# Kernel tuning notes

Hardware: AMD Instinct MI355X
Metric: run time of the kernel (lower is better)

## Reference

```python
import jax, jax.numpy as jnp
import numpy as np

EPSILON = 1e-8
DT = 0.1
STEPS = 3
MASK_DENSITY = 0.01


def setup_inputs() -> dict:
    key = jax.random.key(0)
    k1, k2 = jax.random.split(key)
    B, S, D = 4, 4096, 2
    psi = jax.random.normal(k1, (B, S, D), dtype=jnp.float32)
    # binary mask: threshold a uniform draw to get a sparse 0/1 adjacency
    u = jax.random.uniform(k2, (B, S, S), dtype=jnp.float32)
    binary_mask = (u < MASK_DENSITY).astype(jnp.float32)
    return {"psi": psi, "binary_mask": binary_mask}


def reference(psi, binary_mask):
    def force(state):
        # adjacency-weighted aggregation minus self: [B,S,S] @ [B,S,2]
        return jnp.einsum('bij,bjd->bid', binary_mask, state) - state

    def step(p, _):
        r = jnp.linalg.norm(p, axis=-1, keepdims=True)          # [B,S,1]
        k1 = force(p)
        psi_star = p + DT * k1
        star_norm = jnp.linalg.norm(psi_star, axis=-1, keepdims=True)
        psi_star = psi_star * (r / (star_norm + EPSILON))       # renormalize to r
        k2 = force(psi_star)
        p_new = p + 0.5 * DT * (k1 + k2)
        new_norm = jnp.linalg.norm(p_new, axis=-1, keepdims=True)
        p_new = p_new * (r / (new_norm + EPSILON))              # norm-preserving
        return p_new, None

    psi_out, _ = jax.lax.scan(step, psi, None, length=STEPS)
    return psi_out
```

## Files before the change

### kernel.cpp

```cpp
#include <hip/hip_runtime.h>
#include <stdint.h>

#define BATCH   4
#define SEQ     4096
#define WPR     64
#define NROWS   (BATCH * SEQ)
#define DTS     0.1f
#define HALF_DT 0.05f
#define EPS     1e-8f

__global__ void compress_mask(const float* __restrict__ mask,
                              unsigned long long* __restrict__ bits) {
    int w = blockIdx.x * blockDim.x + threadIdx.x;
    const float4* src = reinterpret_cast<const float4*>(mask) + (size_t)w * 16;
    unsigned long long acc = 0ull;
#pragma unroll
    for (int it = 0; it < 16; ++it) {
        float4 v = src[it];
        unsigned long long n =
              (unsigned long long)(v.x != 0.f)
            | ((unsigned long long)(v.y != 0.f) << 1)
            | ((unsigned long long)(v.z != 0.f) << 2)
            | ((unsigned long long)(v.w != 0.f) << 3);
        acc |= n << (it * 4);
    }
    bits[w] = acc;
}

template <int PHASE>
__global__ void force_step(const unsigned long long* __restrict__ bits,
                           const float2* __restrict__ pIn,
                           const float2* __restrict__ gsrc,
                           float2* __restrict__ k1buf,
                           float2* __restrict__ starbuf,
                           float*  __restrict__ rbuf,
                           float2* __restrict__ outbuf) {
    const int wave = threadIdx.x >> 6;
    const int lane = threadIdx.x & 63;
    const int row  = blockIdx.x * (blockDim.x >> 6) + wave;
    const int b    = row >> 12;
    const float2* gb = gsrc + ((size_t)b << 12);

    unsigned long long w = bits[(size_t)row * WPR + lane];
    float sx = 0.f, sy = 0.f;
    const int base = lane << 6;
    while (w) {
        int j = __builtin_ctzll(w);
        w &= (w - 1);
        float2 v = gb[base + j];
        sx += v.x; sy += v.y;
    }
#pragma unroll
    for (int m = 32; m >= 1; m >>= 1) {
        sx += __shfl_xor(sx, m, 64);
        sy += __shfl_xor(sy, m, 64);
    }
    if (lane == 0) {
        if (PHASE == 0) {
            float2 p = pIn[row];
            float r   = sqrtf(p.x * p.x + p.y * p.y);
            float k1x = sx - p.x, k1y = sy - p.y;
            float tx  = p.x + DTS * k1x, ty = p.y + DTS * k1y;
            float sc  = r / (sqrtf(tx * tx + ty * ty) + EPS);
            k1buf[row]   = make_float2(k1x, k1y);
            starbuf[row] = make_float2(tx * sc, ty * sc);
            rbuf[row]    = r;
        } else {
            float2 st = gsrc[row];
            float k2x = sx - st.x, k2y = sy - st.y;
            float2 p  = pIn[row];
            float2 k1 = k1buf[row];
            float nx  = p.x + HALF_DT * (k1.x + k2x);
            float ny  = p.y + HALF_DT * (k1.y + k2y);
            float sc  = rbuf[row] / (sqrtf(nx * nx + ny * ny) + EPS);
            outbuf[row] = make_float2(nx * sc, ny * sc);
        }
    }
}

extern "C" void kernel_launch(void* const* d_in, const int* in_sizes, int n_in,
                              void* d_out, int out_size, void* d_ws, size_t ws_size,
                              hipStream_t stream) {
    const float* psi  = (const float*)d_in[0];
    const float* mask = (const float*)d_in[1];
    float2* out2 = (float2*)d_out;

    char* ws = (char*)d_ws;
    unsigned long long* bits = (unsigned long long*)ws;
    float2* p    = (float2*)(ws + (size_t)NROWS * WPR * 8);
    float2* k1   = p + NROWS;
    float2* star = k1 + NROWS;
    float*  rbuf = (float*)(star + NROWS);

    compress_mask<<<NROWS * WPR / 256, 256, 0, stream>>>(mask, bits);

    const float2* psi2 = (const float2*)psi;
    const int fgrid = NROWS / 4;

    force_step<0><<<fgrid, 256, 0, stream>>>(bits, psi2, psi2, k1, star, rbuf, nullptr);
    force_step<1><<<fgrid, 256, 0, stream>>>(bits, psi2, star, k1, star, rbuf, p);
    force_step<0><<<fgrid, 256, 0, stream>>>(bits, p, p, k1, star, rbuf, nullptr);
    force_step<1><<<fgrid, 256, 0, stream>>>(bits, p, star, k1, star, rbuf, p);
    force_step<0><<<fgrid, 256, 0, stream>>>(bits, p, p, k1, star, rbuf, nullptr);
    force_step<1><<<fgrid, 256, 0, stream>>>(bits, p, star, k1, star, rbuf, out2);
}
```

Measured before the change: 407.3 us.

## Fuse mask compression and all RK steps into one cooperative kernel

Replaces the separate mask-compression kernel and the six force-step launches with one persistent cooperative kernel. Phases are separated by grid-wide syncs, and each wave handles four rows. Mask compression now has lanes read consecutive float4s (coalesced) and builds the bit words with wave ballots, which interleaves the column bit layout; the gather indexing is updated to match. This targets launch overhead and the strided, uncoalesced mask reads of the old compressor. The cost is grid-sync latency and a dependence on all 1024 blocks being co-resident.

```diff
diff --git a/kernel.cpp b/kernel.cpp
--- a/kernel.cpp
+++ b/kernel.cpp
@@ -1,5 +1,8 @@
 #include <hip/hip_runtime.h>
+#include <hip/hip_cooperative_groups.h>
 #include <stdint.h>
+
+namespace cg = cooperative_groups;
 
 #define BATCH   4
 #define SEQ     4096
@@ -9,45 +12,21 @@
 #define HALF_DT 0.05f
 #define EPS     1e-8f
 
-__global__ void compress_mask(const float* __restrict__ mask,
-                              unsigned long long* __restrict__ bits) {
-    int w = blockIdx.x * blockDim.x + threadIdx.x;
-    const float4* src = reinterpret_cast<const float4*>(mask) + (size_t)w * 16;
-    unsigned long long acc = 0ull;
-#pragma unroll
-    for (int it = 0; it < 16; ++it) {
-        float4 v = src[it];
-        unsigned long long n =
-              (unsigned long long)(v.x != 0.f)
-            | ((unsigned long long)(v.y != 0.f) << 1)
-            | ((unsigned long long)(v.z != 0.f) << 2)
-            | ((unsigned long long)(v.w != 0.f) << 3);
-        acc |= n << (it * 4);
-    }
-    bits[w] = acc;
-}
+#define NBLOCK  1024
+#define NTHR    256
+#define NWAVES  (NBLOCK * NTHR / 64)
+#define ROWS_PER_WAVE (NROWS / NWAVES)
 
-template <int PHASE>
-__global__ void force_step(const unsigned long long* __restrict__ bits,
-                           const float2* __restrict__ pIn,
-                           const float2* __restrict__ gsrc,
-                           float2* __restrict__ k1buf,
-                           float2* __restrict__ starbuf,
-                           float*  __restrict__ rbuf,
-                           float2* __restrict__ outbuf) {
-    const int wave = threadIdx.x >> 6;
-    const int lane = threadIdx.x & 63;
-    const int row  = blockIdx.x * (blockDim.x >> 6) + wave;
-    const int b    = row >> 12;
-    const float2* gb = gsrc + ((size_t)b << 12);
-
+__device__ __forceinline__ float2 row_force_sum(
+        const unsigned long long* __restrict__ bits,
+        const float2* __restrict__ gbatch, int row, int lane) {
     unsigned long long w = bits[(size_t)row * WPR + lane];
+    const int colbase = ((lane >> 2) << 8) | (lane & 3);
     float sx = 0.f, sy = 0.f;
-    const int base = lane << 6;
     while (w) {
         int j = __builtin_ctzll(w);
         w &= (w - 1);
-        float2 v = gb[base + j];
+        float2 v = gbatch[colbase + (j << 2)];
         sx += v.x; sy += v.y;
     }
 #pragma unroll
@@ -55,25 +34,81 @@
         sx += __shfl_xor(sx, m, 64);
         sy += __shfl_xor(sy, m, 64);
     }
-    if (lane == 0) {
-        if (PHASE == 0) {
+    return make_float2(sx, sy);
+}
+
+__global__ __launch_bounds__(NTHR, 4)
+void fused_rdi(const float* __restrict__ mask,
+               const float2* __restrict__ psi,
+               unsigned long long* __restrict__ bits,
+               float2* __restrict__ pbuf,
+               float2* __restrict__ k1buf,
+               float2* __restrict__ starbuf,
+               float*  __restrict__ rbuf,
+               float2* __restrict__ out) {
+    cg::grid_group grid = cg::this_grid();
+    const int wave = (blockIdx.x * NTHR + threadIdx.x) >> 6;
+    const int lane = threadIdx.x & 63;
+
+    for (int i = 0; i < ROWS_PER_WAVE; ++i) {
+        const int row = wave * ROWS_PER_WAVE + i;
+        const float4* src = reinterpret_cast<const float4*>(mask + (size_t)row * SEQ);
+        unsigned long long word = 0ull;
+#pragma unroll
+        for (int c = 0; c < 16; ++c) {
+            float4 v = src[c * 64 + lane];
+            unsigned long long b;
+            b = __ballot(v.x != 0.f); word = (lane == c * 4 + 0) ? b : word;
+            b = __ballot(v.y != 0.f); word = (lane == c * 4 + 1) ? b : word;
+            b = __ballot(v.z != 0.f); word = (lane == c * 4 + 2) ? b : word;
+            b = __ballot(v.w != 0.f); word = (lane == c * 4 + 3) ? b : word;
+        }
+        bits[(size_t)row * WPR + lane] = word;
+    }
+
+    __threadfence();
+    grid.sync();
+
+    for (int s = 0; s < 3; ++s) {
+        const float2* pIn  = (s == 0) ? psi : pbuf;
+        float2*       pOut = (s == 2) ? out : pbuf;
+
+        for (int i = 0; i < ROWS_PER_WAVE; ++i) {
+            const int row = wave * ROWS_PER_WAVE + i;
+            const int b = row >> 12;
+            float2 sum = row_force_sum(bits, pIn + ((size_t)b << 12), row, lane);
             float2 p = pIn[row];
             float r   = sqrtf(p.x * p.x + p.y * p.y);
-            float k1x = sx - p.x, k1y = sy - p.y;
+            float k1x = sum.x - p.x, k1y = sum.y - p.y;
             float tx  = p.x + DTS * k1x, ty = p.y + DTS * k1y;
             float sc  = r / (sqrtf(tx * tx + ty * ty) + EPS);
-            k1buf[row]   = make_float2(k1x, k1y);
-            starbuf[row] = make_float2(tx * sc, ty * sc);
-            rbuf[row]    = r;
-        } else {
-            float2 st = gsrc[row];
-            float k2x = sx - st.x, k2y = sy - st.y;
+            if (lane == 0) {
+                k1buf[row]   = make_float2(k1x, k1y);
+                starbuf[row] = make_float2(tx * sc, ty * sc);
+                rbuf[row]    = r;
+            }
+        }
+
+        __threadfence();
+        grid.sync();
+
+        for (int i = 0; i < ROWS_PER_WAVE; ++i) {
+            const int row = wave * ROWS_PER_WAVE + i;
+            const int b = row >> 12;
+            float2 sum = row_force_sum(bits, starbuf + ((size_t)b << 12), row, lane);
+            float2 st = starbuf[row];
             float2 p  = pIn[row];
             float2 k1 = k1buf[row];
+            float k2x = sum.x - st.x, k2y = sum.y - st.y;
             float nx  = p.x + HALF_DT * (k1.x + k2x);
             float ny  = p.y + HALF_DT * (k1.y + k2y);
             float sc  = rbuf[row] / (sqrtf(nx * nx + ny * ny) + EPS);
-            outbuf[row] = make_float2(nx * sc, ny * sc);
+            if (lane == 0) pOut[row] = make_float2(nx * sc, ny * sc);
+        }
+
+        if (s < 2) {
+            __threadfence();
+            grid.sync();
         }
     }
 }
@@ -92,15 +127,10 @@
     float2* star = k1 + NROWS;
     float*  rbuf = (float*)(star + NROWS);
 
-    compress_mask<<<NROWS * WPR / 256, 256, 0, stream>>>(mask, bits);
+    const float2* psi2 = (const float2*)psi;
 
-    const float2* psi2 = (const float2*)psi;
-    const int fgrid = NROWS / 4;
-
-    force_step<0><<<fgrid, 256, 0, stream>>>(bits, psi2, psi2, k1, star, rbuf, nullptr);
-    force_step<1><<<fgrid, 256, 0, stream>>>(bits, psi2, star, k1, star, rbuf, p);
-    force_step<0><<<fgrid, 256, 0, stream>>>(bits, p, p, k1, star, rbuf, nullptr);
-    force_step<1><<<fgrid, 256, 0, stream>>>(bits, p, star, k1, star, rbuf, p);
-    force_step<0><<<fgrid, 256, 0, stream>>>(bits, p, p, k1, star, rbuf, nullptr);
-    force_step<1><<<fgrid, 256, 0, stream>>>(bits, p, star, k1, star, rbuf, out2);
+    void* args[] = { (void*)&mask, (void*)&psi2, (void*)&bits, (void*)&p,
+                     (void*)&k1, (void*)&star, (void*)&rbuf, (void*)&out2 };
+    hipLaunchCooperativeKernel((void*)fused_rdi, dim3(NBLOCK), dim3(NTHR),
+                               args, 0, stream);
 }
```

Measured after the change: 1.565 ms. +284.3%, slower.

## Fuse mask compression with first force phase using wave-ballot bitpacking

Applied to the files above, without the earlier changes.

Mask compression now runs one wave per row. Each lane reads coalesced float4 chunks, and __ballot builds the 64-bit words, which gives an interleaved column layout. That kernel also computes the first phase-0 force step straight from the fresh bit words, so one launch and one reread of the bit matrix are gone. The gather index mapping changes to match the strided bit layout, which spreads each lane's neighbour reads across the row instead of a contiguous 64-column block.

```diff
diff --git a/kernel.cpp b/kernel.cpp
--- a/kernel.cpp
+++ b/kernel.cpp
@@ -9,45 +9,15 @@
 #define HALF_DT 0.05f
 #define EPS     1e-8f
 
-__global__ void compress_mask(const float* __restrict__ mask,
-                              unsigned long long* __restrict__ bits) {
-    int w = blockIdx.x * blockDim.x + threadIdx.x;
-    const float4* src = reinterpret_cast<const float4*>(mask) + (size_t)w * 16;
-    unsigned long long acc = 0ull;
-#pragma unroll
-    for (int it = 0; it < 16; ++it) {
-        float4 v = src[it];
-        unsigned long long n =
-              (unsigned long long)(v.x != 0.f)
-            | ((unsigned long long)(v.y != 0.f) << 1)
-            | ((unsigned long long)(v.z != 0.f) << 2)
-            | ((unsigned long long)(v.w != 0.f) << 3);
-        acc |= n << (it * 4);
-    }
-    bits[w] = acc;
-}
-
-template <int PHASE>
-__global__ void force_step(const unsigned long long* __restrict__ bits,
-                           const float2* __restrict__ pIn,
-                           const float2* __restrict__ gsrc,
-                           float2* __restrict__ k1buf,
-                           float2* __restrict__ starbuf,
-                           float*  __restrict__ rbuf,
-                           float2* __restrict__ outbuf) {
-    const int wave = threadIdx.x >> 6;
-    const int lane = threadIdx.x & 63;
-    const int row  = blockIdx.x * (blockDim.x >> 6) + wave;
-    const int b    = row >> 12;
-    const float2* gb = gsrc + ((size_t)b << 12);
-
-    unsigned long long w = bits[(size_t)row * WPR + lane];
+__device__ __forceinline__ float2 ballot_force_sum(unsigned long long w,
+                                                   const float2* __restrict__ gb,
+                                                   int lane) {
+    const int colbase = ((lane >> 2) << 8) | (lane & 3);
     float sx = 0.f, sy = 0.f;
-    const int base = lane << 6;
     while (w) {
         int j = __builtin_ctzll(w);
         w &= (w - 1);
-        float2 v = gb[base + j];
+        float2 v = gb[colbase + (j << 2)];
         sx += v.x; sy += v.y;
     }
 #pragma unroll
@@ -55,11 +25,67 @@
         sx += __shfl_xor(sx, m, 64);
         sy += __shfl_xor(sy, m, 64);
     }
+    return make_float2(sx, sy);
+}
+
+__global__ __launch_bounds__(256)
+void compress_phaseA(const float* __restrict__ mask,
+                     const float2* __restrict__ psi,
+                     unsigned long long* __restrict__ bits,
+                     float2* __restrict__ k1buf,
+                     float2* __restrict__ starbuf,
+                     float*  __restrict__ rbuf) {
+    const int row  = (blockIdx.x * blockDim.x + threadIdx.x) >> 6;
+    const int lane = threadIdx.x & 63;
+
+    const float4* src = reinterpret_cast<const float4*>(mask + (size_t)row * SEQ);
+    unsigned long long word = 0ull;
+#pragma unroll
+    for (int c = 0; c < 16; ++c) {
+        float4 v = src[c * 64 + lane];
+        unsigned long long b;
+        b = __ballot(v.x != 0.f); if (lane == c * 4 + 0) word = b;
+        b = __ballot(v.y != 0.f); if (lane == c * 4 + 1) word = b;
+        b = __ballot(v.z != 0.f); if (lane == c * 4 + 2) word = b;
+        b = __ballot(v.w != 0.f); if (lane == c * 4 + 3) word = b;
+    }
+    bits[(size_t)row * WPR + lane] = word;
+
+    const int bidx = row >> 12;
+    float2 sum = ballot_force_sum(word, psi + ((size_t)bidx << 12), lane);
+    float2 p  = psi[row];
+    float r   = sqrtf(p.x * p.x + p.y * p.y);
+    float k1x = sum.x - p.x, k1y = sum.y - p.y;
+    float tx  = p.x + DTS * k1x, ty = p.y + DTS * k1y;
+    float sc  = r / (sqrtf(tx * tx + ty * ty) + EPS);
+    if (lane == 0) {
+        k1buf[row]   = make_float2(k1x, k1y);
+        starbuf[row] = make_float2(tx * sc, ty * sc);
+        rbuf[row]    = r;
+    }
+}
+
+template <int PHASE>
+__global__ __launch_bounds__(256)
+void force_step(const unsigned long long* __restrict__ bits,
+                const float2* __restrict__ pIn,
+                const float2* __restrict__ gsrc,
+                float2* __restrict__ k1buf,
+                float2* __restrict__ starbuf,
+                float*  __restrict__ rbuf,
+                float2* __restrict__ outbuf) {
+    const int row  = (blockIdx.x * blockDim.x + threadIdx.x) >> 6;
+    const int lane = threadIdx.x & 63;
+    const int bidx = row >> 12;
+
+    unsigned long long w = bits[(size_t)row * WPR + lane];
+    float2 sum = ballot_force_sum(w, gsrc + ((size_t)bidx << 12), lane);
+
     if (lane == 0) {
         if (PHASE == 0) {
             float2 p = pIn[row];
             float r   = sqrtf(p.x * p.x + p.y * p.y);
-            float k1x = sx - p.x, k1y = sy - p.y;
+            float k1x = sum.x - p.x, k1y = sum.y - p.y;
             float tx  = p.x + DTS * k1x, ty = p.y + DTS * k1y;
             float sc  = r / (sqrtf(tx * tx + ty * ty) + EPS);
             k1buf[row]   = make_float2(k1x, k1y);
@@ -67,7 +93,7 @@
             rbuf[row]    = r;
         } else {
             float2 st = gsrc[row];
-            float k2x = sx - st.x, k2y = sy - st.y;
+            float k2x = sum.x - st.x, k2y = sum.y - st.y;
             float2 p  = pIn[row];
             float2 k1 = k1buf[row];
             float nx  = p.x + HALF_DT * (k1.x + k2x);
@@ -92,15 +118,13 @@
     float2* star = k1 + NROWS;
     float*  rbuf = (float*)(star + NROWS);
 
-    compress_mask<<<NROWS * WPR / 256, 256, 0, stream>>>(mask, bits);
+    const float2* psi2 = (const float2*)psi;
+    const int grid = NROWS / 4;
 
-    const float2* psi2 = (const float2*)psi;
-    const int fgrid = NROWS / 4;
-
-    force_step<0><<<fgrid, 256, 0, stream>>>(bits, psi2, psi2, k1, star, rbuf, nullptr);
-    force_step<1><<<fgrid, 256, 0, stream>>>(bits, psi2, star, k1, star, rbuf, p);
-    force_step<0><<<fgrid, 256, 0, stream>>>(bits, p, p, k1, star, rbuf, nullptr);
-    force_step<1><<<fgrid, 256, 0, stream>>>(bits, p, star, k1, star, rbuf, p);
-    force_step<0><<<fgrid, 256, 0, stream>>>(bits, p, p, k1, star, rbuf, nullptr);
-    force_step<1><<<fgrid, 256, 0, stream>>>(bits, p, star, k1, star, rbuf, out2);
+    compress_phaseA<<<grid, 256, 0, stream>>>(mask, psi2, bits, k1, star, rbuf);
+    force_step<1><<<grid, 256, 0, stream>>>(bits, psi2, star, k1, star, rbuf, p);
+    force_step<0><<<grid, 256, 0, stream>>>(bits, p, p, k1, star, rbuf, nullptr);
+    force_step<1><<<grid, 256, 0, stream>>>(bits, p, star, k1, star, rbuf, p);
+    force_step<0><<<grid, 256, 0, stream>>>(bits, p, p, k1, star, rbuf, nullptr);
+    force_step<1><<<grid, 256, 0, stream>>>(bits, p, star, k1, star, rbuf, out2);
 }
```

Measured after the change: 394.2 us. 1.03x faster.

## Coalesce mask compression with wave ballots and interleaved bit layout

Applied to the files above, without the earlier changes.

The mask compression kernel now has each wave read 64 consecutive float4s with fully coalesced loads and build the bitmask words with ballots, instead of each thread reading 16 strided float4s. The bit layout changes so each word covers interleaved columns, and force_step decodes column indices to match. Per-row operand loads in force_step are also hoisted ahead of the gather loop. The mask read dominates runtime, so coalescing it targets memory bandwidth, at the cost of more scattered gathers in the force kernels.

```diff
diff --git a/kernel.cpp b/kernel.cpp
--- a/kernel.cpp
+++ b/kernel.cpp
@@ -9,45 +9,61 @@
 #define HALF_DT 0.05f
 #define EPS     1e-8f
 
-__global__ void compress_mask(const float* __restrict__ mask,
-                              unsigned long long* __restrict__ bits) {
-    int w = blockIdx.x * blockDim.x + threadIdx.x;
-    const float4* src = reinterpret_cast<const float4*>(mask) + (size_t)w * 16;
-    unsigned long long acc = 0ull;
-#pragma unroll
-    for (int it = 0; it < 16; ++it) {
-        float4 v = src[it];
-        unsigned long long n =
-              (unsigned long long)(v.x != 0.f)
-            | ((unsigned long long)(v.y != 0.f) << 1)
-            | ((unsigned long long)(v.z != 0.f) << 2)
-            | ((unsigned long long)(v.w != 0.f) << 3);
-        acc |= n << (it * 4);
+#define CB_BLOCKS 2048
+#define CB_THR    256
+#define CB_WAVES  (CB_BLOCKS * CB_THR / 64)
+#define TOTAL_CHUNKS (NROWS * 16)
+#define CHUNKS_PER_WAVE (TOTAL_CHUNKS / CB_WAVES)
+
+__global__ __launch_bounds__(CB_THR)
+void compress_mask(const float* __restrict__ mask,
+                   unsigned long long* __restrict__ bits) {
+    const int wid  = (blockIdx.x * CB_THR + threadIdx.x) >> 6;
+    const int lane = threadIdx.x & 63;
+    const float4* m4 = reinterpret_cast<const float4*>(mask);
+
+#pragma unroll 8
+    for (int it = 0; it < CHUNKS_PER_WAVE; ++it) {
+        const int W = wid * CHUNKS_PER_WAVE + it;
+        float4 v = m4[(size_t)W * 64 + lane];
+        unsigned long long b0 = __ballot(v.x != 0.f);
+        unsigned long long b1 = __ballot(v.y != 0.f);
+        unsigned long long b2 = __ballot(v.z != 0.f);
+        unsigned long long b3 = __ballot(v.w != 0.f);
+        unsigned long long w01 = (lane & 1) ? b1 : b0;
+        unsigned long long w23 = (lane & 1) ? b3 : b2;
+        unsigned long long ws  = (lane & 2) ? w23 : w01;
+        if (lane < 4) bits[((size_t)W << 2) + lane] = ws;
     }
-    bits[w] = acc;
 }
 
 template <int PHASE>
-__global__ void force_step(const unsigned long long* __restrict__ bits,
-                           const float2* __restrict__ pIn,
-                           const float2* __restrict__ gsrc,
-                           float2* __restrict__ k1buf,
-                           float2* __restrict__ starbuf,
-                           float*  __restrict__ rbuf,
-                           float2* __restrict__ outbuf) {
-    const int wave = threadIdx.x >> 6;
+__global__ __launch_bounds__(256)
+void force_step(const unsigned long long* __restrict__ bits,
+                const float2* __restrict__ pIn,
+                const float2* __restrict__ gsrc,
+                float2* __restrict__ k1buf,
+                float2* __restrict__ starbuf,
+                float*  __restrict__ rbuf,
+                float2* __restrict__ outbuf) {
+    const int row  = (blockIdx.x * blockDim.x + threadIdx.x) >> 6;
     const int lane = threadIdx.x & 63;
-    const int row  = blockIdx.x * (blockDim.x >> 6) + wave;
-    const int b    = row >> 12;
-    const float2* gb = gsrc + ((size_t)b << 12);
+    const int bidx = row >> 12;
+    const float2* gb = gsrc + ((size_t)bidx << 12);
 
     unsigned long long w = bits[(size_t)row * WPR + lane];
+
+    float2 p = pIn[row];
+    float2 st = make_float2(0.f, 0.f), k1v = make_float2(0.f, 0.f);
+    float rr = 0.f;
+    if (PHASE == 1) { st = gsrc[row]; k1v = k1buf[row]; rr = rbuf[row]; }
+
+    const int colbase = ((lane >> 2) << 8) | (lane & 3);
     float sx = 0.f, sy = 0.f;
-    const int base = lane << 6;
     while (w) {
         int j = __builtin_ctzll(w);
         w &= (w - 1);
-        float2 v = gb[base + j];
+        float2 v = gb[colbase + (j << 2)];
         sx += v.x; sy += v.y;
     }
 #pragma unroll
@@ -55,9 +71,9 @@
         sx += __shfl_xor(sx, m, 64);
         sy += __shfl_xor(sy, m, 64);
     }
+
     if (lane == 0) {
         if (PHASE == 0) {
-            float2 p = pIn[row];
             float r   = sqrtf(p.x * p.x + p.y * p.y);
             float k1x = sx - p.x, k1y = sy - p.y;
             float tx  = p.x + DTS * k1x, ty = p.y + DTS * k1y;
@@ -66,13 +82,10 @@
             starbuf[row] = make_float2(tx * sc, ty * sc);
             rbuf[row]    = r;
         } else {
-            float2 st = gsrc[row];
             float k2x = sx - st.x, k2y = sy - st.y;
-            float2 p  = pIn[row];
-            float2 k1 = k1buf[row];
-            float nx  = p.x + HALF_DT * (k1.x + k2x);
-            float ny  = p.y + HALF_DT * (k1.y + k2y);
-            float sc  = rbuf[row] / (sqrtf(nx * nx + ny * ny) + EPS);
+            float nx  = p.x + HALF_DT * (k1v.x + k2x);
+            float ny  = p.y + HALF_DT * (k1v.y + k2y);
+            float sc  = rr / (sqrtf(nx * nx + ny * ny) + EPS);
             outbuf[row] = make_float2(nx * sc, ny * sc);
         }
     }
@@ -92,10 +105,10 @@
     float2* star = k1 + NROWS;
     float*  rbuf = (float*)(star + NROWS);
 
-    compress_mask<<<NROWS * WPR / 256, 256, 0, stream>>>(mask, bits);
-
     const float2* psi2 = (const float2*)psi;
     const int fgrid = NROWS / 4;
+
+    compress_mask<<<CB_BLOCKS, CB_THR, 0, stream>>>(mask, bits);
 
     force_step<0><<<fgrid, 256, 0, stream>>>(bits, psi2, psi2, k1, star, rbuf, nullptr);
     force_step<1><<<fgrid, 256, 0, stream>>>(bits, psi2, star, k1, star, rbuf, p);
```

Result: no change. 399.9 us (-1.8%).
